# Kernel tuning notes

Measured on AMD Instinct MI355X. Metric: run time of the kernel, lower is better.

The kernel has to match this reference:

```python
import jax, jax.numpy as jnp
import numpy as np

N_NODES = 50000
N_EDGES = 800000
NFEAT, NHID, NCLASS = 512, 128, 40


def _glorot(key, fan_in, fan_out):
    # mimics the usual GCN uniform init: U(-1/sqrt(fan_out), 1/sqrt(fan_out))
    stdv = 1.0 / np.sqrt(fan_out)
    return jax.random.uniform(key, (fan_in, fan_out), jnp.float32, -stdv, stdv)


def setup_inputs() -> dict:
    key = jax.random.key(0)
    ks = jax.random.split(key, 8)
    x = jax.random.normal(ks[0], (N_NODES, NFEAT), jnp.float32)
    edge_src = jax.random.randint(ks[1], (N_EDGES,), 0, N_NODES)
    edge_dst = jax.random.randint(ks[2], (N_EDGES,), 0, N_NODES)
    edge_weight = jax.random.uniform(ks[3], (N_EDGES,), jnp.float32)
    W1 = _glorot(ks[4], NFEAT, NHID)
    b1 = jnp.zeros((NHID,), jnp.float32)
    W2 = _glorot(ks[5], NHID, NCLASS)
    b2 = jnp.zeros((NCLASS,), jnp.float32)
    return {"x": x, "edge_src": edge_src, "edge_dst": edge_dst,
            "edge_weight": edge_weight, "W1": W1, "b1": b1, "W2": W2, "b2": b2}


def _gcn_layer(x, W, b, edge_src, edge_dst, edge_weight):
    # support = x @ W ; out = spmm(adj, support) + b
    support = x @ W                                   # [N, F_out]
    msgs = support[edge_src] * edge_weight[:, None]   # [E, F_out]
    agg = jax.ops.segment_sum(msgs, edge_dst, num_segments=N_NODES)
    return agg + b


def reference(x, edge_src, edge_dst, edge_weight, W1, b1, W2, b2):
    h = _gcn_layer(x, W1, b1, edge_src, edge_dst, edge_weight)
    h = jax.nn.relu(h)
    # F.dropout(training=False) -> identity in eval mode
    out = _gcn_layer(h, W2, b2, edge_src, edge_dst, edge_weight)
    return out
```

## Files before the change

### kernel.cpp

```cpp
#include <hip/hip_runtime.h>


#define F0 512
#define F1 128
#define F2 40
#define F2P 48

typedef short bf16x8 __attribute__((ext_vector_type(8)));
typedef float f32x4 __attribute__((ext_vector_type(4)));

static __device__ __forceinline__ unsigned short f2b(float f){
    union { float f; unsigned int u; } x; x.f = f;
    unsigned int u = x.u;
    unsigned int r = (u + 0x7fffu + ((u >> 16) & 1u)) >> 16;
    return (unsigned short)r;
}
static __device__ __forceinline__ unsigned short f2b_fast(float f){
    return (unsigned short)((__float_as_uint(f) + 0x8000u) >> 16);
}
static __device__ __forceinline__ unsigned int pack2(float a, float b){
    unsigned int ua = __float_as_uint(a) + 0x8000u;
    unsigned int ub = __float_as_uint(b) + 0x8000u;
    return __builtin_amdgcn_perm(ub, ua, 0x07060302u);
}
static __device__ __forceinline__ bf16x8 pack8(float4 v0, float4 v1){
    union { bf16x8 v; unsigned int d[4]; } r;
    r.d[0] = pack2(v0.x, v0.y);
    r.d[1] = pack2(v0.z, v0.w);
    r.d[2] = pack2(v1.x, v1.y);
    r.d[3] = pack2(v1.z, v1.w);
    return r.v;
}
static __device__ __forceinline__ float b2f(unsigned short h){
    union { unsigned int u; float f; } x; x.u = ((unsigned int)h) << 16; return x.f;
}
static __device__ __forceinline__ unsigned short f2h(float f){
    union { _Float16 h; unsigned short u; } x; x.h = (_Float16)f; return x.u;
}
static __device__ __forceinline__ float h2f(unsigned short u){
    union { unsigned short u; _Float16 h; } x; x.u = u; return (float)x.h;
}

__global__ void prep_w(const float* __restrict__ W1, const float* __restrict__ W2,
                       unsigned short* __restrict__ W1t, unsigned short* __restrict__ W2t,
                       int* __restrict__ cnt8, int n8, int* __restrict__ gflag){
    int idx = blockIdx.x*256 + threadIdx.x;
    if (idx < n8) cnt8[idx] = 0;
    if (idx < 64) gflag[idx] = 0;
    if (idx < F0*F1){
        int k = idx >> 7, n = idx & 127;
        W1t[(size_t)n*F0 + k] = f2b(W1[idx]);
    } else if (idx < F0*F1 + F2P*F1){
        int j = idx - F0*F1;
        int n = j >> 7, k = j & 127;
        float v = (n < F2) ? W2[(size_t)k*F2 + n] : 0.f;
        W2t[j] = f2b(v);
    }
}

__global__ __launch_bounds__(256, 3) void gemm1h(const float* __restrict__ X,
                                                 const unsigned short* __restrict__ W1t,
                                                 unsigned short* __restrict__ S1, int M,
                                                 const int* __restrict__ dst,
                                                 int* __restrict__ cnt8,
                                                 unsigned short* __restrict__ slot,
                                                 int E, int epb){
    __shared__ unsigned short sB[128*136];
    int tid = threadIdx.x;
    int wave = tid >> 6, lane = tid & 63;
    int quad = lane >> 4, l16 = lane & 15;
    int row0 = blockIdx.x * 64;
    int arow = min(row0 + wave*16 + l16, M-1);
    const float* xrow = X + (size_t)arow * F0;

    int eb = blockIdx.x * epb + tid;
    int e0 = eb, e1 = eb+256, e2 = eb+512, e3 = eb+768;
    int d0 = (e0 < E) ? dst[e0] : 0;
    int d1 = (e1 < E) ? dst[e1] : 0;
    int d2 = (e2 < E) ? dst[e2] : 0;
    int d3 = (e3 < E) ? dst[e3] : 0;
    unsigned int sl = 0;

    f32x4 acc[8];
    #pragma unroll
    for (int c=0;c<8;c++) acc[c] = (f32x4){0.f,0.f,0.f,0.f};

    auto stage_b = [&](int p) __attribute__((always_inline)) {
        __syncthreads();
        #pragma unroll
        for (int i=0;i<8;i++){
            int idx = tid + i*256;
            int nn = idx >> 4, c8 = idx & 15;
            *(float4*)&sB[nn*136 + c8*8] =
                *(const float4*)&W1t[(size_t)nn*F0 + p*128 + c8*8];
        }
        __syncthreads();
    };
    auto mfma_ph = [&](int p) __attribute__((always_inline)) {
        #pragma unroll
        for (int s=0;s<4;s++){
            const float* xr = xrow + p*128 + s*32 + quad*8;
            float4 v0 = *(const float4*)(xr);
            float4 v1 = *(const float4*)(xr + 4);
            bf16x8 af = pack8(v0, v1);
            #pragma unroll
            for (int c=0;c<8;c++){
                bf16x8 b = *(bf16x8*)&sB[(c*16 + l16)*136 + s*32 + quad*8];
                acc[c] = __builtin_amdgcn_mfma_f32_16x16x32_bf16(af, b, acc[c], 0, 0, 0);
            }
        }
    };

    stage_b(0);
    if (e0 < E) sl = atomicAdd(&cnt8[d0*8 + (e0 & 7)], 1);
    mfma_ph(0);

    stage_b(1);
    if (e0 < E) slot[e0] = (unsigned short)sl;
    if (e1 < E) sl = atomicAdd(&cnt8[d1*8 + (e1 & 7)], 1);
    mfma_ph(1);

    stage_b(2);
    if (e1 < E) slot[e1] = (unsigned short)sl;
    if (e2 < E) sl = atomicAdd(&cnt8[d2*8 + (e2 & 7)], 1);
    mfma_ph(2);

    stage_b(3);
    if (e2 < E) slot[e2] = (unsigned short)sl;
    if (e3 < E) sl = atomicAdd(&cnt8[d3*8 + (e3 & 7)], 1);
    mfma_ph(3);
    if (e3 < E) slot[e3] = (unsigned short)sl;

    int eend = min(blockIdx.x * epb + epb, E);
    for (int e = eb + 1024; e < eend; e += 256){
        int d = dst[e];
        slot[e] = (unsigned short)atomicAdd(&cnt8[d*8 + (e & 7)], 1);
    }

    #pragma unroll
    for (int c=0;c<8;c++){
        #pragma unroll
        for (int r=0;r<4;r++){
            int grow = row0 + wave*16 + quad*4 + r;
            if (grow < M) S1[(size_t)grow*F1 + c*16 + l16] = f2b_fast(acc[c][r]);
        }
    }
}

__global__ void scan_fused(const int* __restrict__ cnt8, int* __restrict__ offs,
                           int* __restrict__ sbase, int* __restrict__ gflag,
                           int n, int E){
    __shared__ int sd[256];
    __shared__ int s_excl;
    int tid = threadIdx.x, bid = blockIdx.x;
    int base = bid*1024 + tid*4;

    int t[4];
    int lpr[4][8];
    #pragma unroll
    for (int j=0;j<4;j++){
        int node = base+j;
        int tot = 0;
        #pragma unroll
        for (int k=0;k<8;k++) lpr[j][k] = 0;
        if (node < n){
            int4 c0 = *(const int4*)&cnt8[(size_t)node*8];
            int4 c1 = *(const int4*)&cnt8[(size_t)node*8+4];
            int run;
            lpr[j][0] = 0;   run  = c0.x;
            lpr[j][1] = run; run += c0.y;
            lpr[j][2] = run; run += c0.z;
            lpr[j][3] = run; run += c0.w;
            lpr[j][4] = run; run += c1.x;
            lpr[j][5] = run; run += c1.y;
            lpr[j][6] = run; run += c1.z;
            lpr[j][7] = run; run += c1.w;
            tot = run;
        }
        t[j] = tot;
    }
    int v1 = t[0], v2 = t[0]+t[1], v3 = v2+t[2];
    int s = v3 + t[3];
    sd[tid] = s; __syncthreads();
    for (int off=1; off<256; off<<=1){
        int tt = (tid>=off) ? sd[tid-off] : 0;
        __syncthreads();
        sd[tid] += tt;
        __syncthreads();
    }
    int excl = sd[tid] - s;
    int btot = sd[255];

    if (tid == 0)
        __hip_atomic_store(&gflag[bid], btot + 1, __ATOMIC_RELEASE, __HIP_MEMORY_SCOPE_AGENT);
    if (tid < 64){
        int v = 0;
        if (tid < bid){
            int g;
            do {
                g = __hip_atomic_load(&gflag[tid], __ATOMIC_ACQUIRE, __HIP_MEMORY_SCOPE_AGENT);
                if (g == 0) __builtin_amdgcn_s_sleep(1);
            } while (g == 0);
            v = g - 1;
        }
        #pragma unroll
        for (int o=1; o<64; o<<=1) v += __shfl_xor(v, o);
        if (tid == 0) s_excl = v;
    }
    __syncthreads();

    int node_off[4] = {0, v1, v2, v3};
    int gexcl = s_excl + excl;
    #pragma unroll
    for (int j=0;j<4;j++){
        int node = base+j;
        if (node < n){
            int o = gexcl + node_off[j];
            offs[node] = o;
            int4 s0, s1;
            s0.x = o + lpr[j][0]; s0.y = o + lpr[j][1];
            s0.z = o + lpr[j][2]; s0.w = o + lpr[j][3];
            s1.x = o + lpr[j][4]; s1.y = o + lpr[j][5];
            s1.z = o + lpr[j][6]; s1.w = o + lpr[j][7];
            *(int4*)&sbase[(size_t)node*8]   = s0;
            *(int4*)&sbase[(size_t)node*8+4] = s1;
        }
    }
    if (bid == 0 && tid == 0) offs[n] = E;
}

__global__ void scatter_kernel(const int* __restrict__ src, const int* __restrict__ dst,
                               const float* __restrict__ w,
                               const int* __restrict__ sbase,
                               const unsigned short* __restrict__ slot,
                               unsigned int* __restrict__ edges, int E){
    int e = blockIdx.x*256+threadIdx.x;
    if (e<E){
        int d = dst[e];
        int pos = sbase[d*8 + (e & 7)] + (int)slot[e];
        edges[pos] = ((unsigned int)src[e] << 16) | (unsigned int)f2h(w[e]);
    }
}

__global__ void agg1_kernel(const unsigned short* __restrict__ S1, const int* __restrict__ offs,
                            const unsigned int* __restrict__ edges,
                            const float* __restrict__ b1, unsigned short* __restrict__ H, int n){
    int node = blockIdx.x*4 + (threadIdx.x >> 6);
    int lane = threadIdx.x & 63;
    if (node >= n) return;
    int half = lane >> 5, fl = lane & 31;
    int e0 = offs[node], e1 = offs[node+1];
    double a0=0.0, a1=0.0, a2=0.0, a3=0.0;
    int e = e0;
    for (; e+8 <= e1; e += 8){
        unsigned int rA = edges[e   + half];
        unsigned int rB = edges[e+2 + half];
        unsigned int rC = edges[e+4 + half];
        unsigned int rD = edges[e+6 + half];
        ushort4 vA = *(const ushort4*)&S1[((size_t)(rA>>16))*F1 + fl*4];
        ushort4 vB = *(const ushort4*)&S1[((size_t)(rB>>16))*F1 + fl*4];
        ushort4 vC = *(const ushort4*)&S1[((size_t)(rC>>16))*F1 + fl*4];
        ushort4 vD = *(const ushort4*)&S1[((size_t)(rD>>16))*F1 + fl*4];
        double wA = h2f((unsigned short)rA), wB = h2f((unsigned short)rB);
        double wC = h2f((unsigned short)rC), wD = h2f((unsigned short)rD);
        a0 += wA*b2f(vA.x) + wB*b2f(vB.x) + wC*b2f(vC.x) + wD*b2f(vD.x);
        a1 += wA*b2f(vA.y) + wB*b2f(vB.y) + wC*b2f(vC.y) + wD*b2f(vD.y);
        a2 += wA*b2f(vA.z) + wB*b2f(vB.z) + wC*b2f(vC.z) + wD*b2f(vD.z);
        a3 += wA*b2f(vA.w) + wB*b2f(vB.w) + wC*b2f(vC.w) + wD*b2f(vD.w);
    }
    for (; e < e1; e += 2){
        int ee = e + half;
        if (ee < e1){
            unsigned int r = edges[ee];
            ushort4 v = *(const ushort4*)&S1[((size_t)(r>>16))*F1 + fl*4];
            double w = h2f((unsigned short)r);
            a0 += w*b2f(v.x); a1 += w*b2f(v.y); a2 += w*b2f(v.z); a3 += w*b2f(v.w);
        }
    }
    a0 += __shfl_down(a0, 32);
    a1 += __shfl_down(a1, 32);
    a2 += __shfl_down(a2, 32);
    a3 += __shfl_down(a3, 32);
    if (lane < 32){
        float4 bb = *(const float4*)&b1[fl*4];
        float o0 = (float)(a0 + (double)bb.x);
        float o1 = (float)(a1 + (double)bb.y);
        float o2 = (float)(a2 + (double)bb.z);
        float o3 = (float)(a3 + (double)bb.w);
        o0 = o0>0.f?o0:0.f; o1 = o1>0.f?o1:0.f;
        o2 = o2>0.f?o2:0.f; o3 = o3>0.f?o3:0.f;
        union { ushort4 v; unsigned int d[2]; } o;
        o.d[0] = pack2(o0, o1);
        o.d[1] = pack2(o2, o3);
        *(ushort4*)&H[(size_t)node*F1 + fl*4] = o.v;
    }
}

__global__ __launch_bounds__(256) void gemm2_mfma(const unsigned short* __restrict__ H,
                                                  const unsigned short* __restrict__ W2t,
                                                  unsigned short* __restrict__ S2, int M){
    __shared__ unsigned short sB[48][136];
    int tid = threadIdx.x;
    int wave = tid >> 6, lane = tid & 63;
    int quad = lane >> 4, l16 = lane & 15;
    for (int i = tid; i < 48*16; i += 256){
        int nn = i >> 4, p = i & 15;
        *(float4*)&sB[nn][p*8] = *(const float4*)&W2t[(size_t)nn*F1 + p*8];
    }
    int row0 = blockIdx.x * 64;
    int myrow = row0 + wave*16 + l16;
    int arow = min(myrow, M-1);
    const unsigned short* hrow = H + (size_t)arow * F1;
    bf16x8 a[4];
    #pragma unroll
    for (int ks=0; ks<4; ks++) a[ks] = *(const bf16x8*)(hrow + ks*32 + quad*8);
    __syncthreads();
    f32x4 acc[3];
    #pragma unroll
    for (int c=0;c<3;c++) acc[c] = (f32x4){0.f,0.f,0.f,0.f};
    #pragma unroll
    for (int ks=0; ks<4; ks++){
        #pragma unroll
        for (int c=0;c<3;c++){
            bf16x8 b = *(bf16x8*)&sB[c*16 + l16][ks*32 + quad*8];
            acc[c] = __builtin_amdgcn_mfma_f32_16x16x32_bf16(a[ks], b, acc[c], 0, 0, 0);
        }
    }
    #pragma unroll
    for (int c=0;c<3;c++){
        #pragma unroll
        for (int r=0;r<4;r++){
            int grow = row0 + wave*16 + quad*4 + r;
            if (grow < M) S2[(size_t)grow*F2P + c*16 + l16] = f2b_fast(acc[c][r]);
        }
    }
}

__global__ void agg2_kernel(const unsigned short* __restrict__ S2, const int* __restrict__ offs,
                            const unsigned int* __restrict__ edges,
                            const float* __restrict__ b2, float* __restrict__ out, int n){
    int node = blockIdx.x*4 + (threadIdx.x >> 6);
    int lane = threadIdx.x & 63;
    if (node >= n) return;
    int grp = lane >> 4, gl = lane & 15;
    bool act = gl < 10;
    int e0 = offs[node], e1 = offs[node+1];
    double a0=0.0, a1=0.0, a2=0.0, a3=0.0;
    for (int e = e0; e < e1; e += 4){
        int ee = e + grp;
        if (ee < e1 && act){
            unsigned int r = edges[ee];
            ushort4 v = *(const ushort4*)&S2[((size_t)(r>>16))*F2P + gl*4];
            double w = h2f((unsigned short)r);
            a0 += w*b2f(v.x); a1 += w*b2f(v.y); a2 += w*b2f(v.z); a3 += w*b2f(v.w);
        }
    }
    a0 += __shfl_down(a0, 32); a0 += __shfl_down(a0, 16);
    a1 += __shfl_down(a1, 32); a1 += __shfl_down(a1, 16);
    a2 += __shfl_down(a2, 32); a2 += __shfl_down(a2, 16);
    a3 += __shfl_down(a3, 32); a3 += __shfl_down(a3, 16);
    if (lane < 10){
        float4 bb = *(const float4*)&b2[lane*4];
        float4 o;
        o.x = (float)(a0 + (double)bb.x);
        o.y = (float)(a1 + (double)bb.y);
        o.z = (float)(a2 + (double)bb.z);
        o.w = (float)(a3 + (double)bb.w);
        *(float4*)&out[(size_t)node*F2 + lane*4] = o;
    }
}

extern "C" void kernel_launch(void* const* d_in, const int* in_sizes, int n_in,
                              void* d_out, int out_size, void* d_ws, size_t ws_size,
                              hipStream_t stream){
    const float* x    = (const float*)d_in[0];
    const int*   esrc = (const int*)d_in[1];
    const int*   edst = (const int*)d_in[2];
    const float* ew   = (const float*)d_in[3];
    const float* W1   = (const float*)d_in[4];
    const float* b1   = (const float*)d_in[5];
    const float* W2   = (const float*)d_in[6];
    const float* b2   = (const float*)d_in[7];
    float* out = (float*)d_out;
    int N = in_sizes[0] / F0;
    int E = in_sizes[1];

    char* ws = (char*)d_ws;
    size_t off = 0;
    auto alloc = [&](size_t bytes)->void*{
        void* p = ws + off; off += (bytes + 255) & ~(size_t)255; return p;
    };
    unsigned short* S1 = (unsigned short*)alloc(sizeof(unsigned short)*(size_t)N*F1);
    unsigned short* H  = (unsigned short*)alloc(sizeof(unsigned short)*(size_t)N*F1);
    unsigned short* S2 = (unsigned short*)alloc(sizeof(unsigned short)*(size_t)N*F2P);
    unsigned short* W1t = (unsigned short*)alloc(sizeof(unsigned short)*F1*F0);
    unsigned short* W2t = (unsigned short*)alloc(sizeof(unsigned short)*F2P*F1);
    int*   offs  = (int*)alloc(sizeof(int)*(size_t)(N+1));
    int*   cnt8  = (int*)alloc(sizeof(int)*(size_t)N*8);
    int*   sbase = (int*)alloc(sizeof(int)*(size_t)N*8);
    unsigned short* slot = (unsigned short*)alloc(sizeof(unsigned short)*(size_t)E);
    unsigned int* edges = (unsigned int*)alloc(sizeof(unsigned int)*(size_t)E);
    int*   gflag = (int*)alloc(sizeof(int)*64);

    int n8 = N*8;
    int prep_items = n8 > (F0*F1 + F2P*F1) ? n8 : (F0*F1 + F2P*F1);
    prep_w<<<(prep_items+255)/256,256,0,stream>>>(W1, W2, W1t, W2t, cnt8, n8, gflag);

    int gemm_nb = (N+63)/64;
    int epb = (E + gemm_nb - 1) / gemm_nb;
    gemm1h<<<gemm_nb,256,0,stream>>>(x, W1t, S1, N, edst, cnt8, slot, E, epb);

    int nb = (N+1023)/1024;
    scan_fused<<<nb,256,0,stream>>>(cnt8, offs, sbase, gflag, N, E);
    scatter_kernel<<<(E+255)/256,256,0,stream>>>(esrc, edst, ew, sbase, slot, edges, E);

    agg1_kernel<<<(N+3)/4,256,0,stream>>>(S1, offs, edges, b1, H, N);
    gemm2_mfma<<<gemm_nb,256,0,stream>>>(H, W2t, S2, N);
    agg2_kernel<<<(N+3)/4,256,0,stream>>>(S2, offs, edges, b2, out, N);
}
```

Measured before the change: 295.2 us.

## Halve gemm1 row tile and split output columns across wave pairs

```diff
diff --git a/kernel.cpp b/kernel.cpp
--- a/kernel.cpp
+++ b/kernel.cpp
@@ -65,84 +65,79 @@
                                                  int* __restrict__ cnt8,
                                                  unsigned short* __restrict__ slot,
                                                  int E, int epb){
-    __shared__ unsigned short sB[128*136];
+    __shared__ unsigned short sB[128*72];
     int tid = threadIdx.x;
     int wave = tid >> 6, lane = tid & 63;
     int quad = lane >> 4, l16 = lane & 15;
-    int row0 = blockIdx.x * 64;
-    int arow = min(row0 + wave*16 + l16, M-1);
+    int rg = wave >> 1, ch = wave & 1;
+    int row0 = blockIdx.x * 32;
+    int arow = min(row0 + rg*16 + l16, M-1);
     const float* xrow = X + (size_t)arow * F0;
 
     int eb = blockIdx.x * epb + tid;
-    int e0 = eb, e1 = eb+256, e2 = eb+512, e3 = eb+768;
+    int e0 = eb, e1 = eb + 256;
     int d0 = (e0 < E) ? dst[e0] : 0;
     int d1 = (e1 < E) ? dst[e1] : 0;
-    int d2 = (e2 < E) ? dst[e2] : 0;
-    int d3 = (e3 < E) ? dst[e3] : 0;
-    unsigned int sl = 0;
-
-    f32x4 acc[8];
-    #pragma unroll
-    for (int c=0;c<8;c++) acc[c] = (f32x4){0.f,0.f,0.f,0.f};
+    unsigned int sl0 = 0, sl1 = 0;
+
+    f32x4 acc[4];
+    #pragma unroll
+    for (int c=0;c<4;c++) acc[c] = (f32x4){0.f,0.f,0.f,0.f};
 
     auto stage_b = [&](int p) __attribute__((always_inline)) {
         __syncthreads();
         #pragma unroll
-        for (int i=0;i<8;i++){
+        for (int i=0;i<4;i++){
             int idx = tid + i*256;
-            int nn = idx >> 4, c8 = idx & 15;
-            *(float4*)&sB[nn*136 + c8*8] =
-                *(const float4*)&W1t[(size_t)nn*F0 + p*128 + c8*8];
+            int nn = idx >> 3, c8 = idx & 7;
+            *(float4*)&sB[nn*72 + c8*8] =
+                *(const float4*)&W1t[(size_t)nn*F0 + p*64 + c8*8];
         }
         __syncthreads();
     };
     auto mfma_ph = [&](int p) __attribute__((always_inline)) {
         #pragma unroll
-        for (int s=0;s<4;s++){
-            const float* xr = xrow + p*128 + s*32 + quad*8;
+        for (int s=0;s<2;s++){
+            const float* xr = xrow + p*64 + s*32 + quad*8;
             float4 v0 = *(const float4*)(xr);
             float4 v1 = *(const float4*)(xr + 4);
             bf16x8 af = pack8(v0, v1);
             #pragma unroll
-            for (int c=0;c<8;c++){
-                bf16x8 b = *(bf16x8*)&sB[(c*16 + l16)*136 + s*32 + quad*8];
+            for (int c=0;c<4;c++){
+                bf16x8 b = *(bf16x8*)&sB[(ch*64 + c*16 + l16)*72 + s*32 + quad*8];
                 acc[c] = __builtin_amdgcn_mfma_f32_16x16x32_bf16(af, b, acc[c], 0, 0, 0);
             }
         }
     };
 
     stage_b(0);
-    if (e0 < E) sl = atomicAdd(&cnt8[d0*8 + (e0 & 7)], 1);
+    if (e0 < E) sl0 = atomicAdd(&cnt8[d0*8 + (e0 & 7)], 1);
     mfma_ph(0);
-
     stage_b(1);
-    if (e0 < E) slot[e0] = (unsigned short)sl;
-    if (e1 < E) sl = atomicAdd(&cnt8[d1*8 + (e1 & 7)], 1);
+    if (e0 < E) slot[e0] = (unsigned short)sl0;
+    if (e1 < E) sl1 = atomicAdd(&cnt8[d1*8 + (e1 & 7)], 1);
     mfma_ph(1);
-
     stage_b(2);
-    if (e1 < E) slot[e1] = (unsigned short)sl;
-    if (e2 < E) sl = atomicAdd(&cnt8[d2*8 + (e2 & 7)], 1);
+    if (e1 < E) slot[e1] = (unsigned short)sl1;
     mfma_ph(2);
-
-    stage_b(3);
-    if (e2 < E) slot[e2] = (unsigned short)sl;
-    if (e3 < E) sl = atomicAdd(&cnt8[d3*8 + (e3 & 7)], 1);
-    mfma_ph(3);
-    if (e3 < E) slot[e3] = (unsigned short)sl;
+    stage_b(3); mfma_ph(3);
+    stage_b(4); mfma_ph(4);
+    stage_b(5); mfma_ph(5);
+    stage_b(6); mfma_ph(6);
+    stage_b(7); mfma_ph(7);
 
     int eend = min(blockIdx.x * epb + epb, E);
-    for (int e = eb + 1024; e < eend; e += 256){
+    for (int e = eb + 512; e < eend; e += 256){
         int d = dst[e];
         slot[e] = (unsigned short)atomicAdd(&cnt8[d*8 + (e & 7)], 1);
     }
 
     #pragma unroll
-    for (int c=0;c<8;c++){
+    for (int c=0;c<4;c++){
         #pragma unroll
         for (int r=0;r<4;r++){
-            int grow = row0 + wave*16 + quad*4 + r;
-            if (grow < M) S1[(size_t)grow*F1 + c*16 + l16] = f2b_fast(acc[c][r]);
+            int grow = row0 + rg*16 + quad*4 + r;
+            if (grow < M) S1[(size_t)grow*F1 + ch*64 + c*16 + l16] = f2b_fast(acc[c][r]);
         }
     }
 }
@@ -406,15 +401,16 @@
     int prep_items = n8 > (F0*F1 + F2P*F1) ? n8 : (F0*F1 + F2P*F1);
     prep_w<<<(prep_items+255)/256,256,0,stream>>>(W1, W2, W1t, W2t, cnt8, n8, gflag);
 
-    int gemm_nb = (N+63)/64;
-    int epb = (E + gemm_nb - 1) / gemm_nb;
-    gemm1h<<<gemm_nb,256,0,stream>>>(x, W1t, S1, N, edst, cnt8, slot, E, epb);
+    int g1_nb = (N+31)/32;
+    int epb = (E + g1_nb - 1) / g1_nb;
+    gemm1h<<<g1_nb,256,0,stream>>>(x, W1t, S1, N, edst, cnt8, slot, E, epb);
 
     int nb = (N+1023)/1024;
     scan_fused<<<nb,256,0,stream>>>(cnt8, offs, sbase, gflag, N, E);
     scatter_kernel<<<(E+255)/256,256,0,stream>>>(esrc, edst, ew, sbase, slot, edges, E);
 
     agg1_kernel<<<(N+3)/4,256,0,stream>>>(S1, offs, edges, b1, H, N);
-    gemm2_mfma<<<gemm_nb,256,0,stream>>>(H, W2t, S2, N);
+    int gemm2_nb = (N+63)/64;
+    gemm2_mfma<<<gemm2_nb,256,0,stream>>>(H, W2t, S2, N);
     agg2_kernel<<<(N+3)/4,256,0,stream>>>(S2, offs, edges, b2, out, N);
 }
```

Result: slower. 306.4 us (+3.8%).
